# Kernel tuning notes

Hardware: AMD Instinct MI355X
Metric: run time of the kernel (lower is better)

The kernel has to match this reference:

```python
import jax, jax.numpy as jnp
import numpy as np

B, Z, L = 256, 256, 8
C0, H0, W0 = 128, 8, 8
O = C0 * H0 * W0  # 8192


def _conv_transpose(x, w, b):
    """Torch ConvTranspose2d(k=4, s=2, p=1) equivalent.
    w: torch layout (in_ch, out_ch, kH, kW).
    Implemented as lhs-dilated conv with flipped, transposed kernel; pad = k-1-p = 2.
    """
    wt = jnp.flip(w, (2, 3)).transpose(1, 0, 2, 3)  # (out, in, kh, kw)
    y = jax.lax.conv_general_dilated(
        x, wt, window_strides=(1, 1), padding=[(2, 2), (2, 2)],
        lhs_dilation=(2, 2), dimension_numbers=('NCHW', 'OIHW', 'NCHW'))
    return y + b[None, :, None, None]


def setup_inputs() -> dict:
    key = jax.random.key(0)
    ks = jax.random.split(key, 6)
    return {
        'x': jax.random.normal(ks[0], (B, Z), jnp.float32),
        'gw': jax.random.normal(ks[1], (Z, L), jnp.float32) * (2.0 / (Z + L)) ** 0.5,  # xavier_normal
        'gb': jnp.zeros((L,), jnp.float32),
        'pw': jax.random.normal(ks[2], (O, Z, L), jnp.float32) * (1.0 / Z) ** 0.5,  # kaiming linear
        'pb': jnp.zeros((O, L), jnp.float32),
        'w1': jax.random.normal(ks[3], (C0, 64, 4, 4), jnp.float32) * 0.02,
        'b1': jnp.zeros((64,), jnp.float32),
        'w2': jax.random.normal(ks[4], (64, 32, 4, 4), jnp.float32) * 0.02,
        'b2': jnp.zeros((32,), jnp.float32),
        'w3': jax.random.normal(ks[5], (32, 3, 4, 4), jnp.float32) * 0.02,
        'b3': jnp.zeros((3,), jnp.float32),
    }


def reference(x, gw, gb, pw, pb, w1, b1, w2, b2, w3, b3):
    # --- ME mixture of linear experts (linear projection) ---
    g = jax.nn.softmax(x @ gw + gb, axis=1)               # (B, L)
    # Per-expert linear outputs, then gate-weighted sum. Mathematically equal to
    # torch's (pw @ gatings) per-sample weight followed by bmm with x, but avoids
    # the (B, O, Z) intermediate.
    expert_out = jnp.einsum('bi,oil->bol', x, pw)          # (B, O, L)
    out = jnp.einsum('bol,bl->bo', expert_out, g) + g @ pb.T  # (B, O)
    # --- conv-transpose decoder stack ---
    h = out.reshape(B, C0, H0, W0)
    h = jax.nn.relu(_conv_transpose(h, w1, b1))            # (B, 64, 16, 16)
    h = jax.nn.relu(_conv_transpose(h, w2, b2))            # (B, 32, 32, 32)
    h = _conv_transpose(h, w3, b3)                         # (B, 3, 64, 64)
    return h
```

## Files before the change

### kernel.cpp

```cpp
#include <hip/hip_runtime.h>

typedef __bf16 bf16;
typedef __bf16 bf16x8 __attribute__((ext_vector_type(8)));
typedef float f32x4 __attribute__((ext_vector_type(4)));

__device__ __forceinline__ f32x4 mfma16(bf16x8 a, bf16x8 b, f32x4 c) {
  return __builtin_amdgcn_mfma_f32_16x16x32_bf16(a, b, c, 0, 0, 0);
}

__device__ __forceinline__ void gload16(const void* g, void* l) {
  __builtin_amdgcn_global_load_lds(
      (const __attribute__((address_space(1))) void*)g,
      (__attribute__((address_space(3))) void*)(uint32_t)(size_t)l, 16, 0, 0);
}

__device__ __forceinline__ bf16x8 cvt8(float4 a, float4 b) {
  bf16x8 r;
  r[0] = (bf16)a.x; r[1] = (bf16)a.y; r[2] = (bf16)a.z; r[3] = (bf16)a.w;
  r[4] = (bf16)b.x; r[5] = (bf16)b.y; r[6] = (bf16)b.z; r[7] = (bf16)b.w;
  return r;
}

__global__ __launch_bounds__(256) void gating_kernel(
    const float* __restrict__ x, const float* __restrict__ gw,
    const float* __restrict__ gb, bf16* __restrict__ xgbP,
    float* __restrict__ gbuf) {
  const int b = blockIdx.x, tid = threadIdx.x;
  __shared__ float xs[256];
  __shared__ float gs[8];
  xs[tid] = x[b * 256 + tid];
  __syncthreads();
  if (tid < 8) {
    float acc = gb[tid];
    for (int i = 0; i < 256; ++i) acc += xs[i] * gw[i * 8 + tid];
    gs[tid] = acc;
  }
  __syncthreads();
  if (tid == 0) {
    float m = gs[0];
    for (int l = 1; l < 8; ++l) m = fmaxf(m, gs[l]);
    float s = 0.f, e[8];
    for (int l = 0; l < 8; ++l) { e[l] = expf(gs[l] - m); s += e[l]; }
    float inv = 1.f / s;
    for (int l = 0; l < 8; ++l) gs[l] = e[l] * inv;
  }
  __syncthreads();
  if (tid < 8) gbuf[b * 8 + tid] = gs[tid];
  float xv = xs[tid];
  bf16x8 r;
#pragma unroll
  for (int j = 0; j < 8; ++j) r[j] = (bf16)(xv * gs[j]);
  size_t off = (size_t)(b >> 4) * 65536 + (size_t)(tid >> 2) * 1024 +
               (size_t)(((tid & 3) * 16 + (b & 15)) * 16);
  *(bf16x8*)((char*)xgbP + off) = r;
}

template <int CIN, int COUT, int COUTP>
__device__ __forceinline__ void cw_one(const float* __restrict__ w,
                                       bf16* __restrict__ wp, int idx) {
  constexpr int K = 4 * CIN;
  int ic = idx & (CIN - 1);
  int t = (idx / CIN) & 3;
  int oc = (idx / K) % COUTP;
  int p = idx / (K * COUTP);
  bf16 v = (bf16)0.f;
  if (oc < COUT) {
    int py = p >> 1, px = p & 1, tyi = t >> 1, txi = t & 1;
    int ky = py == 0 ? (tyi ? 3 : 1) : (tyi ? 2 : 0);
    int kx = px == 0 ? (txi ? 3 : 1) : (txi ? 2 : 0);
    v = (bf16)w[((ic * COUT + oc) * 4 + ky) * 4 + kx];
  }
  wp[idx] = v;
}

__global__ __launch_bounds__(256) void convert_w_all(
    const float* __restrict__ w1, bf16* __restrict__ w1p,
    const float* __restrict__ w2, bf16* __restrict__ w2p,
    const float* __restrict__ w3, bf16* __restrict__ w3p) {
  int idx = blockIdx.x * 256 + threadIdx.x;
  if (idx < 131072) cw_one<128, 64, 64>(w1, w1p, idx);
  else if (idx < 163840) cw_one<64, 32, 32>(w2, w2p, idx - 131072);
  else if (idx < 172032) cw_one<32, 3, 16>(w3, w3p, idx - 163840);
}

template <int HP, int WP, int C>
__device__ __forceinline__ void bz_one(bf16* __restrict__ buf, int idx) {
  constexpr int NCELL = 2 * WP + 2 * (HP - 2);
  constexpr int C8 = C / 8;
  int c8 = idx % C8;
  int rem = idx / C8;
  int cell = rem % NCELL;
  int b = rem / NCELL;
  int y, x;
  if (cell < WP) { y = 0; x = cell; }
  else if (cell < 2 * WP) { y = HP - 1; x = cell - WP; }
  else { int r2 = cell - 2 * WP; y = 1 + (r2 >> 1); x = (r2 & 1) ? WP - 1 : 0; }
  bf16x8 z = {};
  *(bf16x8*)(buf + ((size_t)(b * HP + y) * WP + x) * C + c8 * 8) = z;
}

__global__ __launch_bounds__(256) void border_zero_all(
    bf16* __restrict__ h0t, bf16* __restrict__ h1, bf16* __restrict__ h2) {
  int idx = blockIdx.x * 256 + threadIdx.x;
  if (idx < 147456) bz_one<10, 10, 128>(h0t, idx);
  else if (idx < 286720) bz_one<18, 18, 64>(h1, idx - 147456);
  else if (idx < 421888) bz_one<34, 34, 32>(h2, idx - 286720);
}

__global__ __launch_bounds__(512) void me_gemm_kernel(
    const float* __restrict__ pw, const bf16* __restrict__ xgbP,
    const float* __restrict__ pb, const float* __restrict__ gbuf,
    bf16* __restrict__ h0t) {
  __shared__ char sA[65536];
  const int tid = threadIdx.x, wv = tid >> 6, l = tid & 63;
  const int lr = l & 15, lkg = l >> 4;
  const int M0 = blockIdx.x * 16;

#pragma unroll
  for (int it = 0; it < 8; ++it) {
    int g = it * 512 + tid;
    int kt = g >> 7, rem = g & 127;
    int row = rem >> 3, ig = rem & 7;
    const float* src = pw + (size_t)(M0 + row) * 2048 + kt * 64 + ig * 8;
    float4 v0 = *(const float4*)src;
    float4 v1 = *(const float4*)(src + 4);
    int L = kt * 2048 + row * 128 + ((ig * 16) ^ ((row & 7) << 4));
    *(bf16x8*)(sA + L) = cvt8(v0, v1);
  }
  __syncthreads();

  int aoff[2];
#pragma unroll
  for (int ks = 0; ks < 2; ++ks)
    aoff[ks] = lr * 128 + (((ks * 4 + lkg) * 16) ^ ((lr & 7) << 4));

  const char* pB0 = (const char*)xgbP + (size_t)(2 * wv) * 65536 + l * 16;
  const char* pB1 = (const char*)xgbP + (size_t)(2 * wv + 1) * 65536 + l * 16;

  f32x4 acc[2] = {};
#pragma unroll 8
  for (int s = 0; s < 64; ++s) {
    const int kt = s >> 1, ks = s & 1;
    const char* base = sA + kt * 2048;
    bf16x8 a0 = *(const bf16x8*)(base + aoff[ks]);
    bf16x8 b0 = *(const bf16x8*)(pB0 + s * 1024);
    bf16x8 b1 = *(const bf16x8*)(pB1 + s * 1024);
    acc[0] = mfma16(a0, b0, acc[0]);
    acc[1] = mfma16(a0, b1, acc[1]);
  }

  float4 g0[2], g1[2];
#pragma unroll
  for (int n = 0; n < 2; ++n) {
    int b = wv * 32 + n * 16 + lr;
    g0[n] = *(const float4*)(gbuf + b * 8);
    g1[n] = *(const float4*)(gbuf + b * 8 + 4);
  }
#pragma unroll
  for (int r = 0; r < 4; ++r) {
    int o = M0 + lkg * 4 + r;
    float4 p0 = *(const float4*)(pb + o * 8);
    float4 p1 = *(const float4*)(pb + o * 8 + 4);
    int cch = o >> 6, y = (o >> 3) & 7, xx = o & 7;
#pragma unroll
    for (int n = 0; n < 2; ++n) {
      int b = wv * 32 + n * 16 + lr;
      float bias = g0[n].x * p0.x + g0[n].y * p0.y + g0[n].z * p0.z + g0[n].w * p0.w +
                   g1[n].x * p1.x + g1[n].y * p1.y + g1[n].z * p1.z + g1[n].w * p1.w;
      h0t[((size_t)(b * 10 + y + 1) * 10 + xx + 1) * 128 + cch] = (bf16)(acc[n][r] + bias);
    }
  }
}

template <int CIN, int H, int YB, int COUTP, int WM, int NF, int SWM, int INIT,
          bool RELU, bool F32OUT, int SIN_SZ>
__global__ __launch_bounds__(256) void convt_kernel(
    const bf16* __restrict__ in, const bf16* __restrict__ wp,
    const float* __restrict__ bias, bf16* __restrict__ out,
    float* __restrict__ fout) {
  constexpr int W = H, WROW = W + 2, ROWB = CIN * 2, GRS = ROWB / 16;
  constexpr int LGR = (GRS == 16) ? 4 : (GRS == 8) ? 3 : 2;
  constexpr int LW = (W == 8) ? 3 : (W == 16) ? 4 : 5;
  constexpr int K = 4 * CIN;
  constexpr int CHUNKS = (YB + 2) * WROW * GRS;
  __shared__ char sIn[SIN_SZ];

  const int tid = threadIdx.x, wv = tid >> 6, l = tid & 63;
  const int nyb = H / YB;
  const int img = blockIdx.x / nyb, y0 = (blockIdx.x % nyb) * YB;

#pragma unroll
  for (int it = 0; it < INIT; ++it) {
    int t = it * 256 + tid;
    int tc = t < CHUNKS ? t : CHUNKS - 1;
    int pix = tc >> LGR, cc = tc & (GRS - 1);
    int ly = pix / WROW, lx = pix % WROW;
    int sb = (cc * 16) ^ ((pix & SWM) << 4);
    gload16(in + ((size_t)((img * (H + 2) + y0 + ly) * (W + 2) + lx)) * CIN + (sb >> 1),
            sIn + it * 4096 + wv * 1024);
  }
  __syncthreads();

  const int lr = l & 15, lkg = l >> 4;
  const int wm = wv & (WM - 1), wn = wv / WM;
  int pcen[2];
#pragma unroll
  for (int m = 0; m < 2; ++m) {
    int r = wm * 32 + m * 16 + lr;
    pcen[m] = ((r >> LW) + 1) * WROW + (r & (W - 1)) + 1;
  }

  f32x4 acc[4][2][NF] = {};
#pragma unroll
  for (int p = 0; p < 4; ++p) {
    const int py = p >> 1, px = p & 1;
#pragma unroll 4
    for (int kk = 0; kk < K; kk += 32) {
      const int t4 = kk / CIN;
      const int tyi = t4 >> 1, txi = t4 & 1;
      const int dy = (py == 0) ? (tyi ? -1 : 0) : (tyi ? 0 : 1);
      const int dx = (px == 0) ? (txi ? -1 : 0) : (txi ? 0 : 1);
      const int icb = (kk % CIN) * 2 + lkg * 16;
      bf16x8 av[2], bv[NF];
#pragma unroll
      for (int m = 0; m < 2; ++m) {
        int pixd = pcen[m] + dy * WROW + dx;
        av[m] = *(const bf16x8*)(sIn + pixd * ROWB + (icb ^ ((pixd & SWM) << 4)));
      }
#pragma unroll
      for (int n = 0; n < NF; ++n) {
        int oc = (wn * NF + n) * 16 + lr;
        bv[n] = *(const bf16x8*)(wp + (size_t)(p * COUTP + oc) * K + kk + lkg * 8);
      }
#pragma unroll
      for (int m = 0; m < 2; ++m)
#pragma unroll
        for (int n = 0; n < NF; ++n) acc[p][m][n] = mfma16(av[m], bv[n], acc[p][m][n]);
    }
  }

#pragma unroll
  for (int p = 0; p < 4; ++p) {
    const int py = p >> 1, px = p & 1;
#pragma unroll
    for (int m = 0; m < 2; ++m)
#pragma unroll
      for (int r4 = 0; r4 < 4; ++r4) {
        int r = wm * 32 + m * 16 + lkg * 4 + r4;
        int yy = r >> LW, xx = r & (W - 1);
        int oy = 2 * (y0 + yy) + py, ox = 2 * xx + px;
#pragma unroll
        for (int n = 0; n < NF; ++n) {
          int oc = (wn * NF + n) * 16 + lr;
          float v = acc[p][m][n][r4];
          if constexpr (F32OUT) {
            if (oc < 3) fout[((size_t)(img * 3 + oc) * (2 * H) + oy) * (2 * H) + ox] = v + bias[oc];
          } else {
            v += bias[oc];
            if constexpr (RELU) v = fmaxf(v, 0.f);
            out[((size_t)(img * (2 * H + 2) + oy + 1) * (2 * H + 2) + ox + 1) * COUTP + oc] = (bf16)v;
          }
        }
      }
  }
}

extern "C" void kernel_launch(void* const* d_in, const int* in_sizes, int n_in,
                              void* d_out, int out_size, void* d_ws, size_t ws_size,
                              hipStream_t stream) {
  const float* x  = (const float*)d_in[0];
  const float* gw = (const float*)d_in[1];
  const float* gb = (const float*)d_in[2];
  const float* pw = (const float*)d_in[3];
  const float* pb = (const float*)d_in[4];
  const float* w1 = (const float*)d_in[5];
  const float* b1 = (const float*)d_in[6];
  const float* w2 = (const float*)d_in[7];
  const float* b2 = (const float*)d_in[8];
  const float* w3 = (const float*)d_in[9];
  const float* b3 = (const float*)d_in[10];
  float* outp = (float*)d_out;

  char* ws = (char*)d_ws;
  bf16*  xgbP = (bf16*)(ws + 0);
  float* gbuf = (float*)(ws + 1048576);
  bf16*  h0t  = (bf16*)(ws + 1056768);
  bf16*  w1p  = (bf16*)(ws + 7610368);
  bf16*  h1   = (bf16*)(ws + 7872512);
  bf16*  w2p  = (bf16*)(ws + 18489344);
  bf16*  h2   = (bf16*)(ws + 18554880);
  bf16*  w3p  = (bf16*)(ws + 37494784);

  border_zero_all<<<1648, 256, 0, stream>>>(h0t, h1, h2);
  gating_kernel<<<256, 256, 0, stream>>>(x, gw, gb, xgbP, gbuf);
  convert_w_all<<<672, 256, 0, stream>>>(w1, w1p, w2, w2p, w3, w3p);

  me_gemm_kernel<<<512, 512, 0, stream>>>(pw, xgbP, pb, gbuf, h0t);

  convt_kernel<128, 8, 8, 64, 2, 2, 7, 7, true, false, 28672>
      <<<256, 256, 0, stream>>>(h0t, w1p, b1, h1, nullptr);
  convt_kernel<64, 16, 8, 32, 4, 2, 7, 6, true, false, 24576>
      <<<512, 256, 0, stream>>>(h1, w2p, b2, h2, nullptr);
  convt_kernel<32, 32, 4, 16, 4, 1, 3, 4, false, true, 16384>
      <<<2048, 256, 0, stream>>>(h2, w3p, b3, nullptr, outp);
}
```

Baseline: 124.5 us.

## Retile expert GEMM to stream A from global with wider N tiles; shrink conv tiles

The expert-projection GEMM no longer stages the fp32 weight tile in LDS. Each 128-thread block now handles 32 output rows and each wave covers 128 batch columns, loading and converting A directly from global memory with 16 accumulators per lane. This removes the LDS staging and barrier and reuses each A load across eight B tiles, at the cost of high register pressure and fewer, smaller blocks (256 blocks of 2 waves). The first two conv-transpose launches also switch to smaller row blocks and fewer warp tiles, doubling grid size to raise parallelism.

```diff
diff --git a/kernel.cpp b/kernel.cpp
--- a/kernel.cpp
+++ b/kernel.cpp
@@ -107,69 +107,53 @@
   else if (idx < 421888) bz_one<34, 34, 32>(h2, idx - 286720);
 }
 
-__global__ __launch_bounds__(512) void me_gemm_kernel(
+__global__ __launch_bounds__(128, 1) void me_gemm_kernel(
     const float* __restrict__ pw, const bf16* __restrict__ xgbP,
     const float* __restrict__ pb, const float* __restrict__ gbuf,
     bf16* __restrict__ h0t) {
-  __shared__ char sA[65536];
   const int tid = threadIdx.x, wv = tid >> 6, l = tid & 63;
   const int lr = l & 15, lkg = l >> 4;
-  const int M0 = blockIdx.x * 16;
-
-#pragma unroll
-  for (int it = 0; it < 8; ++it) {
-    int g = it * 512 + tid;
-    int kt = g >> 7, rem = g & 127;
-    int row = rem >> 3, ig = rem & 7;
-    const float* src = pw + (size_t)(M0 + row) * 2048 + kt * 64 + ig * 8;
-    float4 v0 = *(const float4*)src;
-    float4 v1 = *(const float4*)(src + 4);
-    int L = kt * 2048 + row * 128 + ((ig * 16) ^ ((row & 7) << 4));
-    *(bf16x8*)(sA + L) = cvt8(v0, v1);
-  }
-  __syncthreads();
-
-  int aoff[2];
-#pragma unroll
-  for (int ks = 0; ks < 2; ++ks)
-    aoff[ks] = lr * 128 + (((ks * 4 + lkg) * 16) ^ ((lr & 7) << 4));
-
-  const char* pB0 = (const char*)xgbP + (size_t)(2 * wv) * 65536 + l * 16;
-  const char* pB1 = (const char*)xgbP + (size_t)(2 * wv + 1) * 65536 + l * 16;
-
-  f32x4 acc[2] = {};
+  const int M0 = blockIdx.x * 32;
+
+  const float* pA0 = pw + (size_t)(M0 + lr) * 2048 + lkg * 8;
+  const float* pA1 = pA0 + 16 * 2048;
+  const char* pB = (const char*)xgbP + (size_t)(8 * wv) * 65536 + l * 16;
+
+  f32x4 acc[2][8] = {};
 #pragma unroll 8
   for (int s = 0; s < 64; ++s) {
-    const int kt = s >> 1, ks = s & 1;
-    const char* base = sA + kt * 2048;
-    bf16x8 a0 = *(const bf16x8*)(base + aoff[ks]);
-    bf16x8 b0 = *(const bf16x8*)(pB0 + s * 1024);
-    bf16x8 b1 = *(const bf16x8*)(pB1 + s * 1024);
-    acc[0] = mfma16(a0, b0, acc[0]);
-    acc[1] = mfma16(a0, b1, acc[1]);
-  }
-
-  float4 g0[2], g1[2];
-#pragma unroll
-  for (int n = 0; n < 2; ++n) {
-    int b = wv * 32 + n * 16 + lr;
-    g0[n] = *(const float4*)(gbuf + b * 8);
-    g1[n] = *(const float4*)(gbuf + b * 8 + 4);
-  }
-#pragma unroll
-  for (int r = 0; r < 4; ++r) {
-    int o = M0 + lkg * 4 + r;
-    float4 p0 = *(const float4*)(pb + o * 8);
-    float4 p1 = *(const float4*)(pb + o * 8 + 4);
-    int cch = o >> 6, y = (o >> 3) & 7, xx = o & 7;
-#pragma unroll
-    for (int n = 0; n < 2; ++n) {
-      int b = wv * 32 + n * 16 + lr;
-      float bias = g0[n].x * p0.x + g0[n].y * p0.y + g0[n].z * p0.z + g0[n].w * p0.w +
-                   g1[n].x * p1.x + g1[n].y * p1.y + g1[n].z * p1.z + g1[n].w * p1.w;
-      h0t[((size_t)(b * 10 + y + 1) * 10 + xx + 1) * 128 + cch] = (bf16)(acc[n][r] + bias);
+    float4 a00 = *(const float4*)(pA0 + s * 32);
+    float4 a01 = *(const float4*)(pA0 + s * 32 + 4);
+    float4 a10 = *(const float4*)(pA1 + s * 32);
+    float4 a11 = *(const float4*)(pA1 + s * 32 + 4);
+    bf16x8 a0 = cvt8(a00, a01);
+    bf16x8 a1 = cvt8(a10, a11);
+#pragma unroll
+    for (int j = 0; j < 8; ++j) {
+      bf16x8 bv = *(const bf16x8*)(pB + (size_t)j * 65536 + s * 1024);
+      acc[0][j] = mfma16(a0, bv, acc[0][j]);
+      acc[1][j] = mfma16(a1, bv, acc[1][j]);
     }
   }
+
+#pragma unroll
+  for (int m = 0; m < 2; ++m)
+#pragma unroll
+    for (int r = 0; r < 4; ++r) {
+      int o = M0 + m * 16 + lkg * 4 + r;
+      float4 p0 = *(const float4*)(pb + o * 8);
+      float4 p1 = *(const float4*)(pb + o * 8 + 4);
+      int cch = o >> 6, y = (o >> 3) & 7, xx = o & 7;
+#pragma unroll
+      for (int j = 0; j < 8; ++j) {
+        int b = (8 * wv + j) * 16 + lr;
+        const float* gr = gbuf + b * 8;
+        float bias = gr[0] * p0.x + gr[1] * p0.y + gr[2] * p0.z + gr[3] * p0.w +
+                     gr[4] * p1.x + gr[5] * p1.y + gr[6] * p1.z + gr[7] * p1.w;
+        h0t[((size_t)(b * 10 + y + 1) * 10 + xx + 1) * 128 + cch] =
+            (bf16)(acc[m][j][r] + bias);
+      }
+    }
 }
 
 template <int CIN, int H, int YB, int COUTP, int WM, int NF, int SWM, int INIT,
@@ -295,12 +279,12 @@
   gating_kernel<<<256, 256, 0, stream>>>(x, gw, gb, xgbP, gbuf);
   convert_w_all<<<672, 256, 0, stream>>>(w1, w1p, w2, w2p, w3, w3p);
 
-  me_gemm_kernel<<<512, 512, 0, stream>>>(pw, xgbP, pb, gbuf, h0t);
-
-  convt_kernel<128, 8, 8, 64, 2, 2, 7, 7, true, false, 28672>
-      <<<256, 256, 0, stream>>>(h0t, w1p, b1, h1, nullptr);
-  convt_kernel<64, 16, 8, 32, 4, 2, 7, 6, true, false, 24576>
-      <<<512, 256, 0, stream>>>(h1, w2p, b2, h2, nullptr);
+  me_gemm_kernel<<<256, 128, 0, stream>>>(pw, xgbP, pb, gbuf, h0t);
+
+  convt_kernel<128, 8, 4, 64, 1, 1, 7, 4, true, false, 16384>
+      <<<512, 256, 0, stream>>>(h0t, w1p, b1, h1, nullptr);
+  convt_kernel<64, 16, 4, 32, 2, 1, 7, 4, true, false, 16384>
+      <<<1024, 256, 0, stream>>>(h1, w2p, b2, h2, nullptr);
   convt_kernel<32, 32, 4, 16, 4, 1, 3, 4, false, true, 16384>
       <<<2048, 256, 0, stream>>>(h2, w3p, b3, nullptr, outp);
 }
```

Result: slower. 164.6 us (+32.3%).
